# Kernel tuning notes

Hardware: AMD Instinct MI355X
Metric: run time of the kernel (lower is better)

Reference implementation:

```python
import jax, jax.numpy as jnp
import numpy as np

B, S, D, H, M = 4, 2048, 1024, 16, 128
DH = D // H
SCALE = jnp.float32(np.sqrt(D / H))


def setup_inputs() -> dict:
    key = jax.random.key(0)
    ks = jax.random.split(key, 4)
    x = jax.random.normal(ks[0], (B, S, D), dtype=jnp.float32)
    mask = jnp.zeros((B, 1, 1, S), dtype=bool)
    W_in = jax.random.normal(ks[1], (3 * D, D), dtype=jnp.float32) * 0.02
    b_in = jnp.zeros((3 * D,), dtype=jnp.float32)
    pos_emb = jax.random.normal(ks[2], (2 * M + 1, DH), dtype=jnp.float32)
    W_out = jax.random.normal(ks[3], (D, D), dtype=jnp.float32) * 0.02
    b_out = jnp.zeros((D,), dtype=jnp.float32)
    return {"x": x, "mask": mask, "W_in": W_in, "b_in": b_in,
            "pos_emb": pos_emb, "W_out": W_out, "b_out": b_out}


def _arrange_pos(pos_emb, seq_len, max_len):
    k = jnp.arange(seq_len)
    q = jnp.arange(seq_len)
    idx = jnp.clip(k[None, :] - q[:, None], -max_len, max_len) + max_len  # [S,S]
    return pos_emb[idx]  # [S,S,DH]


def reference(x, mask, W_in, b_in, pos_emb, W_out, b_out):
    b, s, d = x.shape
    qkv = x @ W_in.T + b_in                      # [B,S,3D]
    qkv = qkv.reshape(b, s, H, 3 * DH).transpose(0, 2, 1, 3)  # [B,H,S,3DH]
    Q, K, V = jnp.split(qkv, 3, axis=3)          # each [B,H,S,DH]
    logits = jnp.einsum('bhqd,bhkd->bhqk', Q, K)
    rel = _arrange_pos(pos_emb, s, M)            # [S,S,DH] (q,k,dh)
    pos_logits = jnp.einsum('bhqd,qkd->bhqk', Q, rel)
    logits = (logits + pos_logits) / SCALE
    logits = jnp.where(mask, -jnp.inf, logits)
    attn = jax.nn.softmax(logits, axis=3)
    combined = jnp.einsum('bhqk,bhkd->bhqd', attn, V)
    out = combined.transpose(0, 2, 1, 3).reshape(b, s, d)  # concat heads
    return out @ W_out.T + b_out
```

## Files before the change

### kernel.cpp

```cpp
#include <hip/hip_runtime.h>
#include <hip/hip_bf16.h>
#include <math.h>

#define SS 2048
#define HH 16
#define NPOS 257
#define C_SCALE 0.18033688f
#define DTHR 8.0f

typedef short  s16x8 __attribute__((ext_vector_type(8)));
typedef float  f32x4 __attribute__((ext_vector_type(4)));
typedef unsigned u32x4 __attribute__((ext_vector_type(4)));

__device__ __forceinline__ unsigned short f2bf(float f) {
    unsigned u = __builtin_bit_cast(unsigned, f);
    u += 0x7fff + ((u >> 16) & 1);
    return (unsigned short)(u >> 16);
}
__device__ __forceinline__ float bf2f(unsigned short b) {
    return __builtin_bit_cast(float, (unsigned)b << 16);
}
__device__ __forceinline__ s16x8 pack8(float4 a, float4 b) {
    s16x8 v;
    v[0]=(short)f2bf(a.x); v[1]=(short)f2bf(a.y); v[2]=(short)f2bf(a.z); v[3]=(short)f2bf(a.w);
    v[4]=(short)f2bf(b.x); v[5]=(short)f2bf(b.y); v[6]=(short)f2bf(b.z); v[7]=(short)f2bf(b.w);
    return v;
}
__device__ __forceinline__ unsigned cvtpk(float lo, float hi) {
    unsigned r;
    asm("v_cvt_pk_bf16_f32 %0, %1, %2" : "=v"(r) : "v"(lo), "v"(hi));
    return r;
}
__device__ __forceinline__ float exp2_fast(float x) {
    float r;
    asm("v_exp_f32 %0, %1" : "=v"(r) : "v"(x));
    return r;
}
__device__ __forceinline__ f32x4 mfma16(s16x8 a, s16x8 b, f32x4 c) {
    return __builtin_amdgcn_mfma_f32_16x16x32_bf16(a, b, c, 0, 0, 0);
}
__device__ __forceinline__ void gload_lds16(const void* gsrc, void* ldst) {
    __builtin_amdgcn_global_load_lds(
        (const __attribute__((address_space(1))) unsigned int*)gsrc,
        (__attribute__((address_space(3))) unsigned int*)ldst,
        16, 0, 0);
}
__device__ __forceinline__ int colp(int k) {
    return ((k >> 5) << 6) | (((k >> 2) & 3) << 4) | (((k >> 4) & 1) << 3) | ((k & 3) << 1);
}

__global__ __launch_bounds__(256)
void cvt_bf16(const float* __restrict__ in, unsigned short* __restrict__ out, int n8)
{
    for (int i = blockIdx.x * blockDim.x + threadIdx.x; i < n8; i += gridDim.x * blockDim.x) {
        const float4* p = (const float4*)(in + (size_t)i * 8);
        *(s16x8*)(out + (size_t)i * 8) = pack8(p[0], p[1]);
    }
}

__global__ __launch_bounds__(256)
void gemm_bf16_nt(const unsigned short* __restrict__ A,
                  const unsigned short* __restrict__ Bm,
                  const float* __restrict__ bias, void* __restrict__ Cout,
                  int Ndim, int Kdim, int out_bf16)
{
    __shared__ short As[128 * 32];
    __shared__ short Bs[128 * 32];
    const int tid  = threadIdx.x;
    const int lane = tid & 63;
    const int wv   = tid >> 6;
    const int g    = lane >> 4;
    const int ln   = lane & 15;
    const int wm   = wv >> 1, wn = wv & 1;
    const int tm   = blockIdx.y << 7, tn = blockIdx.x << 7;
    const int srow  = lane >> 2;
    const int sslot = lane & 3;

    f32x4 acc[4][4];
#pragma unroll
    for (int mi = 0; mi < 4; ++mi)
#pragma unroll
        for (int ni = 0; ni < 4; ++ni) acc[mi][ni] = f32x4{0.f, 0.f, 0.f, 0.f};

    const unsigned short* Ab = A  + (size_t)(tm + wv*32 + srow) * Kdim + sslot*8;
    const unsigned short* Bb = Bm + (size_t)(tn + wv*32 + srow) * Kdim + sslot*8;
    const size_t rstep16 = (size_t)16 * Kdim;
    char* lA = (char*)As + (wv*32) * 64;
    char* lB = (char*)Bs + (wv*32) * 64;

    for (int k0 = 0; k0 < Kdim; k0 += 32) {
        __syncthreads();
        gload_lds16(Ab + k0,           lA);
        gload_lds16(Ab + k0 + rstep16, lA + 1024);
        gload_lds16(Bb + k0,           lB);
        gload_lds16(Bb + k0 + rstep16, lB + 1024);
        __syncthreads();

        s16x8 af[4], bf_[4];
#pragma unroll
        for (int mi = 0; mi < 4; ++mi)
            af[mi] = *(const s16x8*)((char*)As + (wm*64 + mi*16 + ln)*64 + g*16);
#pragma unroll
        for (int ni = 0; ni < 4; ++ni)
            bf_[ni] = *(const s16x8*)((char*)Bs + (wn*64 + ni*16 + ln)*64 + g*16);
#pragma unroll
        for (int mi = 0; mi < 4; ++mi)
#pragma unroll
            for (int ni = 0; ni < 4; ++ni)
                acc[mi][ni] = mfma16(af[mi], bf_[ni], acc[mi][ni]);
    }

#pragma unroll
    for (int ni = 0; ni < 4; ++ni) {
        const int col = tn + wn*64 + ni*16 + ln;
        const float bcol = bias[col];
#pragma unroll
        for (int mi = 0; mi < 4; ++mi) {
#pragma unroll
            for (int j = 0; j < 4; ++j) {
                const int row = tm + wm*64 + mi*16 + 4*g + j;
                const float v = acc[mi][ni][j] + bcol;
                if (out_bf16) ((unsigned short*)Cout)[(size_t)row * Ndim + col] = f2bf(v);
                else          ((float*)Cout)[(size_t)row * Ndim + col] = v;
            }
        }
    }
}

#define FAR_LDS  32768
#define NEAR_LDS (32768 + 64*260*2)

#define QKT_STEP(kbp)                                                         \
    f32x4 sA[4], sB[4];                                                       \
    _Pragma("unroll")                                                         \
    for (int t = 0; t < 4; ++t) { sA[t] = f32x4{0,0,0,0}; sB[t] = f32x4{0,0,0,0}; } \
    __builtin_amdgcn_s_setprio(1);                                            \
    _Pragma("unroll")                                                         \
    for (int kc = 0; kc < 2; ++kc) {                                          \
        s16x8 kf[4];                                                          \
        _Pragma("unroll")                                                     \
        for (int t = 0; t < 4; ++t)                                           \
            kf[t] = *(const s16x8*)((kbp) + (t*16 + ln)*128 + ((kc*64 + g*16) ^ swz)); \
        _Pragma("unroll")                                                     \
        for (int t = 0; t < 4; ++t) {                                         \
            sA[t] = mfma16(kf[t], qfA[kc], sA[t]);                            \
            sB[t] = mfma16(kf[t], qfB[kc], sB[t]);                            \
        }                                                                     \
    }                                                                         \
    __builtin_amdgcn_s_setprio(0);

#define SOFTMAX_AV(vbp)                                                       \
    {                                                                         \
        float mxA = sA[0][0], mxB = sB[0][0];                                 \
        _Pragma("unroll")                                                     \
        for (int t = 0; t < 4; ++t)                                           \
            _Pragma("unroll")                                                 \
            for (int j = 0; j < 4; ++j) {                                     \
                mxA = fmaxf(mxA, sA[t][j]); mxB = fmaxf(mxB, sB[t][j]);       \
            }                                                                 \
        if (__any(fmaxf(mxA - mA, mxB - mB) > DTHR)) {                        \
            float mrA = mxA, mrB = mxB;                                       \
            mrA = fmaxf(mrA, __shfl_xor(mrA, 16, 64));                        \
            mrA = fmaxf(mrA, __shfl_xor(mrA, 32, 64));                        \
            mrB = fmaxf(mrB, __shfl_xor(mrB, 16, 64));                        \
            mrB = fmaxf(mrB, __shfl_xor(mrB, 32, 64));                        \
            const float nmA = fmaxf(mA, mrA), nmB = fmaxf(mB, mrB);           \
            const float cA = exp2_fast(mA - nmA), cB = exp2_fast(mB - nmB);   \
            mA = nmA; mB = nmB;                                               \
            _Pragma("unroll")                                                 \
            for (int j = 0; j < 4; ++j) {                                     \
                const int src = (lane & 48) + 4*g + j;                        \
                const float aj = __shfl(cA, src, 64), bj = __shfl(cB, src, 64); \
                _Pragma("unroll")                                             \
                for (int dt = 0; dt < 4; ++dt) { oA[dt][j] *= aj; oB[dt][j] *= bj; } \
                lA[j] *= aj; lB[j] *= bj;                                     \
            }                                                                 \
        }                                                                     \
        u32x4 paA[2], paB[2];                                                 \
        _Pragma("unroll")                                                     \
        for (int t = 0; t < 4; ++t) {                                         \
            const float a0 = exp2_fast(sA[t][0] - mA), a1 = exp2_fast(sA[t][1] - mA); \
            const float a2 = exp2_fast(sA[t][2] - mA), a3 = exp2_fast(sA[t][3] - mA); \
            const float b0 = exp2_fast(sB[t][0] - mB), b1 = exp2_fast(sB[t][1] - mB); \
            const float b2 = exp2_fast(sB[t][2] - mB), b3 = exp2_fast(sB[t][3] - mB); \
            paA[t>>1][2*(t&1)]   = cvtpk(a0, a1);                             \
            paA[t>>1][2*(t&1)+1] = cvtpk(a2, a3);                             \
            paB[t>>1][2*(t&1)]   = cvtpk(b0, b1);                             \
            paB[t>>1][2*(t&1)+1] = cvtpk(b2, b3);                             \
        }                                                                     \
        __builtin_amdgcn_s_setprio(1);                                        \
        _Pragma("unroll")                                                     \
        for (int kc = 0; kc < 2; ++kc) {                                      \
            const s16x8 pA_ = __builtin_bit_cast(s16x8, paA[kc]);             \
            const s16x8 pB_ = __builtin_bit_cast(s16x8, paB[kc]);             \
            _Pragma("unroll")                                                 \
            for (int dt = 0; dt < 4; ++dt) {                                  \
                const s16x8 bv = *(const s16x8*)((vbp) + (dt*16 + ln)*128 + ((kc*64 + g*16) ^ swz)); \
                oA[dt] = mfma16(pA_, bv, oA[dt]);                             \
                oB[dt] = mfma16(pB_, bv, oB[dt]);                             \
            }                                                                 \
            lA = mfma16(pA_, ONES, lA);                                       \
            lB = mfma16(pB_, ONES, lB);                                       \
        }                                                                     \
        __builtin_amdgcn_s_setprio(0);                                        \
    }

#define WRITE_V_PAIR(vb_, vlo, vhi, dbase)                                    \
    _Pragma("unroll")                                                         \
    for (int c_ = 0; c_ < 8; ++c_) {                                          \
        const int d_ = (dbase) + c_;                                          \
        const unsigned pv_ = (unsigned)(unsigned short)(vlo)[c_] |            \
                             ((unsigned)(unsigned short)(vhi)[c_] << 16);     \
        *(unsigned*)((vb_) + d_*128 + (vcp ^ ((d_&7)<<4))) = pv_;             \
    }

__global__ __launch_bounds__(256, 3)
void attn_far(const unsigned short* __restrict__ qkv,
              const float* __restrict__ pos_emb,
              float* __restrict__ o_state,
              float* __restrict__ m_state,
              float* __restrict__ l_state)
{
    extern __shared__ char smem[];
    char* ksb = smem;
    char* vtb = smem + 16384;

    const int tid = threadIdx.x, lane = tid & 63, wv = tid >> 6;
    const int g = lane >> 4, ln = lane & 15;
    const int fid = ((blockIdx.x & 7) << 7) | (blockIdx.x >> 3);
    const int q0 = (fid & 15) << 7, h = (fid >> 4) & 15, b = fid >> 8;
    const size_t base = ((size_t)b * SS) * 3072 + (size_t)h * 192;
    const int q0w = q0 + wv*32;
    const int swz = (ln & 7) << 4;

    s16x8 qfA[2], qfB[2];
    {
        const unsigned short* qp = qkv + base + (size_t)(q0w + ln) * 3072;
        qfA[0] = *(const s16x8*)(qp + g*8);
        qfA[1] = *(const s16x8*)(qp + 32 + g*8);
        qp += (size_t)16 * 3072;
        qfB[0] = *(const s16x8*)(qp + g*8);
        qfB[1] = *(const s16x8*)(qp + 32 + g*8);
    }

    const int kdof = 8*((lane & 7) ^ (lane >> 3));
    const unsigned short* kgp0 = qkv + base + 64 + (size_t)(16*wv + (lane>>3)) * 3072 + kdof;
    const unsigned short* kgp1 = kgp0 + (size_t)8*3072;
    char* kld = ksb + wv*2048;
    const int vs  = tid & 31;
    const int vdc = (tid >> 5) << 3;
    const int vcp = colp(2*vs);
    const unsigned short* vg0 = qkv + base + 128 + (size_t)(2*vs) * 3072 + vdc;
    const unsigned short* vg1 = vg0 + 3072;
    s16x8 vK0, vK1;

#define F_ISSUE_K(kt, buf) do {                                               \
        gload_lds16(kgp0 + (size_t)(kt)*(64*3072), kld + (buf)*8192);         \
        gload_lds16(kgp1 + (size_t)(kt)*(64*3072), kld + (buf)*8192 + 1024); } while (0)
#define F_ISSUE_V(kt) do {                                                    \
        vK0 = *(const s16x8*)(vg0 + (size_t)(kt)*(64*3072));                  \
        vK1 = *(const s16x8*)(vg1 + (size_t)(kt)*(64*3072)); } while (0)

    const int ktA = max(0, (q0 - 128) >> 6);
    const int ktB = min(32, (q0 + 256) >> 6);
    const int gap = ktB - ktA, nfar = 32 - gap;

    {
        const int kt0 = (0 < ktA) ? 0 : gap;
        F_ISSUE_K(kt0, 0);
        F_ISSUE_V(kt0);
    }

    float bloA, bhiA, bloB, bhiB;
    {
        const int bsrc = (ln >> 2) << 4;
#pragma unroll
        for (int pass = 0; pass < 2; ++pass) {
            const int c  = pass*256 + ln;
            const int cc = c > 256 ? 256 : c;
            const float* pp = pos_emb + (size_t)cc * 64 + 8*g;
            s16x8 b0 = pack8(((const float4*)pp)[0], ((const float4*)(pp+4))[0]);
            s16x8 b1 = pack8(((const float4*)(pp+32))[0], ((const float4*)(pp+36))[0]);
            f32x4 dA = {0,0,0,0}, dB = {0,0,0,0};
            dA = mfma16(qfA[0], b0, dA); dA = mfma16(qfA[1], b1, dA);
            dB = mfma16(qfB[0], b0, dB); dB = mfma16(qfB[1], b1, dB);
            const int s3 = ln & 3;
            float vA_ = __shfl(dA[0]*C_SCALE, bsrc, 64);
            float vA1 = __shfl(dA[1]*C_SCALE, bsrc, 64);
            float vA2 = __shfl(dA[2]*C_SCALE, bsrc, 64);
            float vA3 = __shfl(dA[3]*C_SCALE, bsrc, 64);
            float rA = s3 == 0 ? vA_ : s3 == 1 ? vA1 : s3 == 2 ? vA2 : vA3;
            float vB_ = __shfl(dB[0]*C_SCALE, bsrc, 64);
            float vB1 = __shfl(dB[1]*C_SCALE, bsrc, 64);
            float vB2 = __shfl(dB[2]*C_SCALE, bsrc, 64);
            float vB3 = __shfl(dB[3]*C_SCALE, bsrc, 64);
            float rB = s3 == 0 ? vB_ : s3 == 1 ? vB1 : s3 == 2 ? vB2 : vB3;
            if (pass == 0) { bloA = rA; bloB = rB; } else { bhiA = rA; bhiB = rB; }
        }
    }

    WRITE_V_PAIR(vtb, vK0, vK1, vdc)
    __syncthreads();

    f32x4 oA[4], oB[4], lA = {0,0,0,0}, lB = {0,0,0,0};
#pragma unroll
    for (int dt = 0; dt < 4; ++dt) { oA[dt] = f32x4{0,0,0,0}; oB[dt] = f32x4{0,0,0,0}; }
    float mA = -INFINITY, mB = -INFINITY;
    s16x8 ONES;
#pragma unroll
    for (int i = 0; i < 8; ++i) ONES[i] = (short)0x3F80;

    for (int v = 0; v < nfar; ++v) {
        const int kt = (v < ktA) ? v : v + gap;
        const char* kbp = ksb + (v & 1)*8192;
        const char* vbp = vtb + (v & 1)*8192;
        if (v + 1 < nfar) {
            const int ktn = (v + 1 < ktA) ? v + 1 : v + 1 + gap;
            F_ISSUE_K(ktn, (v + 1) & 1);
            F_ISSUE_V(ktn);
        }

        QKT_STEP(kbp)

        const float bcA = (kt < ktA) ? bloA : bhiA;
        const float bcB = (kt < ktA) ? bloB : bhiB;
#pragma unroll
        for (int t = 0; t < 4; ++t)
#pragma unroll
            for (int j = 0; j < 4; ++j) {
                sA[t][j] = sA[t][j]*C_SCALE + bcA;
                sB[t][j] = sB[t][j]*C_SCALE + bcB;
            }

        SOFTMAX_AV(vbp)

        if (v + 1 < nfar) WRITE_V_PAIR(vtb + ((v+1)&1)*8192, vK0, vK1, vdc)
        __syncthreads();
    }

    const size_t rbase = (((size_t)(b*HH + h)) << 11) + q0w;
    if (lane < 16)      m_state[rbase + ln] = mA;
    else if (lane < 32) m_state[rbase + 16 + ln] = mB;
    if (ln == 0) {
#pragma unroll
        for (int j = 0; j < 4; ++j) l_state[rbase + 4*g + j] = lA[j];
    } else if (ln == 1) {
#pragma unroll
        for (int j = 0; j < 4; ++j) l_state[rbase + 16 + 4*g + j] = lB[j];
    }
#pragma unroll
    for (int dt = 0; dt < 4; ++dt)
#pragma unroll
        for (int j = 0; j < 4; ++j) {
            o_state[(rbase + 4*g + j)*64 + dt*16 + ln]      = oA[dt][j];
            o_state[(rbase + 16 + 4*g + j)*64 + dt*16 + ln] = oB[dt][j];
        }
}

__global__ __launch_bounds__(128)
void attn_near(const unsigned short* __restrict__ qkv,
               const float* __restrict__ pos_emb,
               const float* __restrict__ o_state,
               const float* __restrict__ m_state,
               const float* __restrict__ l_state,
               unsigned short* __restrict__ comb)
{
    extern __shared__ char smem[];
    char* ksb = smem;
    char* vtb = smem + 16384;
    unsigned short* tab = (unsigned short*)(smem + 32768);

    const int tid = threadIdx.x, lane = tid & 63, wv = tid >> 6;
    const int g = lane >> 4, ln = lane & 15;
    const int fid = ((blockIdx.x & 7) << 8) | (blockIdx.x >> 3);
    const int q0 = (fid & 31) << 6, h = (fid >> 5) & 15, b = fid >> 9;
    const size_t base = ((size_t)b * SS) * 3072 + (size_t)h * 192;
    const int q0w = q0 + wv*32;
    const int swz = (ln & 7) << 4;

    s16x8 qfA[2], qfB[2];
    {
        const unsigned short* qp = qkv + base + (size_t)(q0w + ln) * 3072;
        qfA[0] = *(const s16x8*)(qp + g*8);
        qfA[1] = *(const s16x8*)(qp + 32 + g*8);
        qp += (size_t)16 * 3072;
        qfB[0] = *(const s16x8*)(qp + g*8);
        qfB[1] = *(const s16x8*)(qp + 32 + g*8);
    }

    const int kdof = 8*((lane & 7) ^ (lane >> 3));
    const unsigned short* kgpN = qkv + base + 64 + (size_t)(32*wv + (lane>>3)) * 3072 + kdof;
    char* kldN = ksb + wv*4096;
    const int vs  = tid & 31;
    const int vdc = (tid >> 5) << 3;
    const int vcp = colp(2*vs);
    const unsigned short* vg0 = qkv + base + 128 + (size_t)(2*vs) * 3072 + vdc;
    const unsigned short* vg1 = vg0 + 3072;
    s16x8 vA0, vA1, vB0, vB1;

#define N_ISSUE_K(kt, buf) do {                                               \
        _Pragma("unroll")                                                     \
        for (int gs = 0; gs < 4; ++gs)                                        \
            gload_lds16(kgpN + (size_t)(kt)*(64*3072) + (size_t)gs*(8*3072),  \
                        kldN + (buf)*8192 + gs*1024); } while (0)
#define N_ISSUE_V(kt) do {                                                    \
        vA0 = *(const s16x8*)(vg0 + (size_t)(kt)*(64*3072));                  \
        vA1 = *(const s16x8*)(vg1 + (size_t)(kt)*(64*3072));                  \
        vB0 = *(const s16x8*)(vg0 + (size_t)(kt)*(64*3072) + 32);             \
        vB1 = *(const s16x8*)(vg1 + (size_t)(kt)*(64*3072) + 32); } while (0)
#define N_WRITE_V(buf) do {                                                   \
        char* vb_ = vtb + (buf)*8192;                                         \
        WRITE_V_PAIR(vb_, vA0, vA1, vdc)                                      \
        WRITE_V_PAIR(vb_, vB0, vB1, vdc + 32)                                 \
    } while (0)

    const int q0p = q0 & ~127;
    const int ktA = max(0, (q0p - 128) >> 6);
    const int ktB = min(32, (q0p + 256) >> 6);
    const int ntile = ktB - ktA;

    N_ISSUE_K(ktA, 0);
    N_ISSUE_V(ktA);

    for (int ct = 0; ct < 17; ++ct) {
        const int c  = ct*16 + ln;
        const int cc = c > 256 ? 256 : c;
        const float* pp = pos_emb + (size_t)cc * 64 + 8*g;
        s16x8 b0 = pack8(((const float4*)pp)[0], ((const float4*)(pp+4))[0]);
        s16x8 b1 = pack8(((const float4*)(pp+32))[0], ((const float4*)(pp+36))[0]);
        f32x4 dA = {0,0,0,0}, dB = {0,0,0,0};
        dA = mfma16(qfA[0], b0, dA); dA = mfma16(qfA[1], b1, dA);
        dB = mfma16(qfB[0], b0, dB); dB = mfma16(qfB[1], b1, dB);
        if (c < NPOS) {
#pragma unroll
            for (int j = 0; j < 4; ++j) {
                tab[(32*wv + 4*g + j)*260 + c]      = f2bf(dA[j] * C_SCALE);
                tab[(32*wv + 16 + 4*g + j)*260 + c] = f2bf(dB[j] * C_SCALE);
            }
        }
    }

    N_WRITE_V(0);
    __syncthreads();

    const size_t rbase = (((size_t)(b*HH + h)) << 11) + q0w;
    float mA = m_state[rbase + ln];
    float mB = m_state[rbase + 16 + ln];
    f32x4 lA, lB;
#pragma unroll
    for (int j = 0; j < 4; ++j) {
        lA[j] = l_state[rbase + 4*g + j];
        lB[j] = l_state[rbase + 16 + 4*g + j];
    }
    f32x4 oA[4], oB[4];
#pragma unroll
    for (int dt = 0; dt < 4; ++dt)
#pragma unroll
        for (int j = 0; j < 4; ++j) {
            oA[dt][j] = o_state[(rbase + 4*g + j)*64 + dt*16 + ln];
            oB[dt][j] = o_state[(rbase + 16 + 4*g + j)*64 + dt*16 + ln];
        }

    const int rowA = (32*wv + ln)*260, rowB = rowA + 16*260;
    const int coffA = 4*g - 32*wv - ln + 128 - q0;
    const int coffB = coffA - 16;
    s16x8 ONES;
#pragma unroll
    for (int i = 0; i < 8; ++i) ONES[i] = (short)0x3F80;

    for (int v = 0; v < ntile; ++v) {
        const int kt = ktA + v;
        const char* kbp = ksb + (v & 1)*8192;
        const char* vbp = vtb + (v & 1)*8192;
        if (v + 1 < ntile) { N_ISSUE_K(kt + 1, (v + 1) & 1); N_ISSUE_V(kt + 1); }

        QKT_STEP(kbp)

        const int kb0 = kt << 6;
#pragma unroll
        for (int t = 0; t < 4; ++t)
#pragma unroll
            for (int j = 0; j < 4; ++j) {
                int cA = kb0 + 16*t + j + coffA;
                cA = cA < 0 ? 0 : (cA > 256 ? 256 : cA);
                int cB = kb0 + 16*t + j + coffB;
                cB = cB < 0 ? 0 : (cB > 256 ? 256 : cB);
                sA[t][j] = sA[t][j]*C_SCALE + bf2f(tab[rowA + cA]);
                sB[t][j] = sB[t][j]*C_SCALE + bf2f(tab[rowB + cB]);
            }

        SOFTMAX_AV(vbp)

        if (v + 1 < ntile) N_WRITE_V((v + 1) & 1);
        __syncthreads();
    }

    f32x4 ivA, ivB;
#pragma unroll
    for (int j = 0; j < 4; ++j) { ivA[j] = 1.0f / lA[j]; ivB[j] = 1.0f / lB[j]; }
#pragma unroll
    for (int dt = 0; dt < 4; ++dt)
#pragma unroll
        for (int j = 0; j < 4; ++j) {
            comb[((size_t)b*SS + q0w + 4*g + j)*1024 + h*64 + dt*16 + ln] =
                f2bf(oA[dt][j] * ivA[j]);
            comb[((size_t)b*SS + q0w + 16 + 4*g + j)*1024 + h*64 + dt*16 + ln] =
                f2bf(oB[dt][j] * ivB[j]);
        }
}

extern "C" void kernel_launch(void* const* d_in, const int* in_sizes, int n_in,
                              void* d_out, int out_size, void* d_ws, size_t ws_size,
                              hipStream_t stream)
{
    const float* x     = (const float*)d_in[0];
    const float* W_in  = (const float*)d_in[2];
    const float* b_in  = (const float*)d_in[3];
    const float* pos   = (const float*)d_in[4];
    const float* W_out = (const float*)d_in[5];
    const float* b_out = (const float*)d_in[6];
    float* out = (float*)d_out;

    char* ws = (char*)d_ws;
    unsigned short* qkv_bf  = (unsigned short*)(ws);
    unsigned short* comb_bf = (unsigned short*)(ws +  50331648);
    unsigned short* x_bf    = (unsigned short*)(ws +  67108864);
    unsigned short* wi_bf   = (unsigned short*)(ws +  83886080);
    unsigned short* wo_bf   = (unsigned short*)(ws +  90177536);
    float*          o_state = (float*)        (ws +  92274688);
    float*          m_state = (float*)        (ws + 125829120);
    float*          l_state = (float*)        (ws + 126353408);

    cvt_bf16<<<2048, 256, 0, stream>>>(x,     x_bf,  8192*1024/8);
    cvt_bf16<<<1024, 256, 0, stream>>>(W_in,  wi_bf, 3072*1024/8);
    cvt_bf16<<<512,  256, 0, stream>>>(W_out, wo_bf, 1024*1024/8);

    gemm_bf16_nt<<<dim3(24, 64), 256, 0, stream>>>(x_bf, wi_bf, b_in, qkv_bf, 3072, 1024, 1);

    (void)hipFuncSetAttribute((const void*)attn_far,
                              hipFuncAttributeMaxDynamicSharedMemorySize, FAR_LDS);
    attn_far<<<dim3(1024), 256, FAR_LDS, stream>>>(qkv_bf, pos, o_state, m_state, l_state);

    (void)hipFuncSetAttribute((const void*)attn_near,
                              hipFuncAttributeMaxDynamicSharedMemorySize, NEAR_LDS);
    attn_near<<<dim3(2048), 128, NEAR_LDS, stream>>>(qkv_bf, pos, o_state, m_state, l_state, comb_bf);

    gemm_bf16_nt<<<dim3(8, 64), 256, 0, stream>>>(comb_bf, wo_bf, b_out, (void*)out, 1024, 1024, 0);
}
```

Measured before the change: 300.0 us.

## Rebalance attention warps: far kernel 64 rows/warp, near kernel 16 rows/warp

The far-attention kernel now runs 2 waves per block, each owning 64 query rows (four 16-row groups). Each K/V fragment loaded from LDS is therefore reused across four MFMA groups, and each wave issues four K loads and four V loads. The near kernel goes the other way: 4 waves per block with 16 rows each, which lowers register pressure and the per-wave work inside the band. The trade-off is higher register use and lower occupancy in the far kernel (launch bounds 128,2) in exchange for better LDS reuse, plus more waves per block and more synchronization in the near kernel.

```diff
diff --git a/kernel.cpp b/kernel.cpp
--- a/kernel.cpp
+++ b/kernel.cpp
@@ -130,81 +130,6 @@
 #define FAR_LDS  32768
 #define NEAR_LDS (32768 + 64*260*2)
 
-#define QKT_STEP(kbp)                                                         \
-    f32x4 sA[4], sB[4];                                                       \
-    _Pragma("unroll")                                                         \
-    for (int t = 0; t < 4; ++t) { sA[t] = f32x4{0,0,0,0}; sB[t] = f32x4{0,0,0,0}; } \
-    __builtin_amdgcn_s_setprio(1);                                            \
-    _Pragma("unroll")                                                         \
-    for (int kc = 0; kc < 2; ++kc) {                                          \
-        s16x8 kf[4];                                                          \
-        _Pragma("unroll")                                                     \
-        for (int t = 0; t < 4; ++t)                                           \
-            kf[t] = *(const s16x8*)((kbp) + (t*16 + ln)*128 + ((kc*64 + g*16) ^ swz)); \
-        _Pragma("unroll")                                                     \
-        for (int t = 0; t < 4; ++t) {                                         \
-            sA[t] = mfma16(kf[t], qfA[kc], sA[t]);                            \
-            sB[t] = mfma16(kf[t], qfB[kc], sB[t]);                            \
-        }                                                                     \
-    }                                                                         \
-    __builtin_amdgcn_s_setprio(0);
-
-#define SOFTMAX_AV(vbp)                                                       \
-    {                                                                         \
-        float mxA = sA[0][0], mxB = sB[0][0];                                 \
-        _Pragma("unroll")                                                     \
-        for (int t = 0; t < 4; ++t)                                           \
-            _Pragma("unroll")                                                 \
-            for (int j = 0; j < 4; ++j) {                                     \
-                mxA = fmaxf(mxA, sA[t][j]); mxB = fmaxf(mxB, sB[t][j]);       \
-            }                                                                 \
-        if (__any(fmaxf(mxA - mA, mxB - mB) > DTHR)) {                        \
-            float mrA = mxA, mrB = mxB;                                       \
-            mrA = fmaxf(mrA, __shfl_xor(mrA, 16, 64));                        \
-            mrA = fmaxf(mrA, __shfl_xor(mrA, 32, 64));                        \
-            mrB = fmaxf(mrB, __shfl_xor(mrB, 16, 64));                        \
-            mrB = fmaxf(mrB, __shfl_xor(mrB, 32, 64));                        \
-            const float nmA = fmaxf(mA, mrA), nmB = fmaxf(mB, mrB);           \
-            const float cA = exp2_fast(mA - nmA), cB = exp2_fast(mB - nmB);   \
-            mA = nmA; mB = nmB;                                               \
-            _Pragma("unroll")                                                 \
-            for (int j = 0; j < 4; ++j) {                                     \
-                const int src = (lane & 48) + 4*g + j;                        \
-                const float aj = __shfl(cA, src, 64), bj = __shfl(cB, src, 64); \
-                _Pragma("unroll")                                             \
-                for (int dt = 0; dt < 4; ++dt) { oA[dt][j] *= aj; oB[dt][j] *= bj; } \
-                lA[j] *= aj; lB[j] *= bj;                                     \
-            }                                                                 \
-        }                                                                     \
-        u32x4 paA[2], paB[2];                                                 \
-        _Pragma("unroll")                                                     \
-        for (int t = 0; t < 4; ++t) {                                         \
-            const float a0 = exp2_fast(sA[t][0] - mA), a1 = exp2_fast(sA[t][1] - mA); \
-            const float a2 = exp2_fast(sA[t][2] - mA), a3 = exp2_fast(sA[t][3] - mA); \
-            const float b0 = exp2_fast(sB[t][0] - mB), b1 = exp2_fast(sB[t][1] - mB); \
-            const float b2 = exp2_fast(sB[t][2] - mB), b3 = exp2_fast(sB[t][3] - mB); \
-            paA[t>>1][2*(t&1)]   = cvtpk(a0, a1);                             \
-            paA[t>>1][2*(t&1)+1] = cvtpk(a2, a3);                             \
-            paB[t>>1][2*(t&1)]   = cvtpk(b0, b1);                             \
-            paB[t>>1][2*(t&1)+1] = cvtpk(b2, b3);                             \
-        }                                                                     \
-        __builtin_amdgcn_s_setprio(1);                                        \
-        _Pragma("unroll")                                                     \
-        for (int kc = 0; kc < 2; ++kc) {                                      \
-            const s16x8 pA_ = __builtin_bit_cast(s16x8, paA[kc]);             \
-            const s16x8 pB_ = __builtin_bit_cast(s16x8, paB[kc]);             \
-            _Pragma("unroll")                                                 \
-            for (int dt = 0; dt < 4; ++dt) {                                  \
-                const s16x8 bv = *(const s16x8*)((vbp) + (dt*16 + ln)*128 + ((kc*64 + g*16) ^ swz)); \
-                oA[dt] = mfma16(pA_, bv, oA[dt]);                             \
-                oB[dt] = mfma16(pB_, bv, oB[dt]);                             \
-            }                                                                 \
-            lA = mfma16(pA_, ONES, lA);                                       \
-            lB = mfma16(pB_, ONES, lB);                                       \
-        }                                                                     \
-        __builtin_amdgcn_s_setprio(0);                                        \
-    }
-
 #define WRITE_V_PAIR(vb_, vlo, vhi, dbase)                                    \
     _Pragma("unroll")                                                         \
     for (int c_ = 0; c_ < 8; ++c_) {                                          \
@@ -214,7 +139,7 @@
         *(unsigned*)((vb_) + d_*128 + (vcp ^ ((d_&7)<<4))) = pv_;             \
     }
 
-__global__ __launch_bounds__(256, 3)
+__global__ __launch_bounds__(128, 2)
 void attn_far(const unsigned short* __restrict__ qkv,
               const float* __restrict__ pos_emb,
               float* __restrict__ o_state,
@@ -230,36 +155,42 @@
     const int fid = ((blockIdx.x & 7) << 7) | (blockIdx.x >> 3);
     const int q0 = (fid & 15) << 7, h = (fid >> 4) & 15, b = fid >> 8;
     const size_t base = ((size_t)b * SS) * 3072 + (size_t)h * 192;
-    const int q0w = q0 + wv*32;
+    const int q0w = q0 + wv*64;
     const int swz = (ln & 7) << 4;
 
-    s16x8 qfA[2], qfB[2];
-    {
-        const unsigned short* qp = qkv + base + (size_t)(q0w + ln) * 3072;
-        qfA[0] = *(const s16x8*)(qp + g*8);
-        qfA[1] = *(const s16x8*)(qp + 32 + g*8);
-        qp += (size_t)16 * 3072;
-        qfB[0] = *(const s16x8*)(qp + g*8);
-        qfB[1] = *(const s16x8*)(qp + 32 + g*8);
+    s16x8 qf[4][2];
+#pragma unroll
+    for (int gg = 0; gg < 4; ++gg) {
+        const unsigned short* qp = qkv + base + (size_t)(q0w + 16*gg + ln) * 3072;
+        qf[gg][0] = *(const s16x8*)(qp + g*8);
+        qf[gg][1] = *(const s16x8*)(qp + 32 + g*8);
     }
 
     const int kdof = 8*((lane & 7) ^ (lane >> 3));
-    const unsigned short* kgp0 = qkv + base + 64 + (size_t)(16*wv + (lane>>3)) * 3072 + kdof;
-    const unsigned short* kgp1 = kgp0 + (size_t)8*3072;
-    char* kld = ksb + wv*2048;
+    const unsigned short* kgp0 = qkv + base + 64 + (size_t)(32*wv + (lane>>3)) * 3072 + kdof;
+    char* kld = ksb + wv*4096;
     const int vs  = tid & 31;
     const int vdc = (tid >> 5) << 3;
     const int vcp = colp(2*vs);
     const unsigned short* vg0 = qkv + base + 128 + (size_t)(2*vs) * 3072 + vdc;
     const unsigned short* vg1 = vg0 + 3072;
-    s16x8 vK0, vK1;
+    s16x8 vK0, vK1, vK2, vK3;
 
 #define F_ISSUE_K(kt, buf) do {                                               \
-        gload_lds16(kgp0 + (size_t)(kt)*(64*3072), kld + (buf)*8192);         \
-        gload_lds16(kgp1 + (size_t)(kt)*(64*3072), kld + (buf)*8192 + 1024); } while (0)
+        _Pragma("unroll")                                                     \
+        for (int gs = 0; gs < 4; ++gs)                                        \
+            gload_lds16(kgp0 + (size_t)(kt)*(64*3072) + (size_t)gs*(8*3072),  \
+                        kld + (buf)*8192 + gs*1024); } while (0)
 #define F_ISSUE_V(kt) do {                                                    \
-        vK0 = *(const s16x8*)(vg0 + (size_t)(kt)*(64*3072));                  \
-        vK1 = *(const s16x8*)(vg1 + (size_t)(kt)*(64*3072)); } while (0)
+        const unsigned short* v0_ = vg0 + (size_t)(kt)*(64*3072);             \
+        const unsigned short* v1_ = vg1 + (size_t)(kt)*(64*3072);             \
+        vK0 = *(const s16x8*)(v0_);      vK1 = *(const s16x8*)(v1_);          \
+        vK2 = *(const s16x8*)(v0_ + 32); vK3 = *(const s16x8*)(v1_ + 32); } while (0)
+#define F_WRITE_V(buf) do {                                                   \
+        char* vb_ = vtb + (buf)*8192;                                         \
+        WRITE_V_PAIR(vb_, vK0, vK1, vdc)                                      \
+        WRITE_V_PAIR(vb_, vK2, vK3, vdc + 32)                                 \
+    } while (0)
 
     const int ktA = max(0, (q0 - 128) >> 6);
     const int ktB = min(32, (q0 + 256) >> 6);
@@ -271,9 +202,10 @@
         F_ISSUE_V(kt0);
     }
 
-    float bloA, bhiA, bloB, bhiB;
+    float blo[4], bhi[4];
     {
         const int bsrc = (ln >> 2) << 4;
+        const int s3 = ln & 3;
 #pragma unroll
         for (int pass = 0; pass < 2; ++pass) {
             const int c  = pass*256 + ln;
@@ -281,31 +213,32 @@
             const float* pp = pos_emb + (size_t)cc * 64 + 8*g;
             s16x8 b0 = pack8(((const float4*)pp)[0], ((const float4*)(pp+4))[0]);
             s16x8 b1 = pack8(((const float4*)(pp+32))[0], ((const float4*)(pp+36))[0]);
-            f32x4 dA = {0,0,0,0}, dB = {0,0,0,0};
-            dA = mfma16(qfA[0], b0, dA); dA = mfma16(qfA[1], b1, dA);
-            dB = mfma16(qfB[0], b0, dB); dB = mfma16(qfB[1], b1, dB);
-            const int s3 = ln & 3;
-            float vA_ = __shfl(dA[0]*C_SCALE, bsrc, 64);
-            float vA1 = __shfl(dA[1]*C_SCALE, bsrc, 64);
-            float vA2 = __shfl(dA[2]*C_SCALE, bsrc, 64);
-            float vA3 = __shfl(dA[3]*C_SCALE, bsrc, 64);
-            float rA = s3 == 0 ? vA_ : s3 == 1 ? vA1 : s3 == 2 ? vA2 : vA3;
-            float vB_ = __shfl(dB[0]*C_SCALE, bsrc, 64);
-            float vB1 = __shfl(dB[1]*C_SCALE, bsrc, 64);
-            float vB2 = __shfl(dB[2]*C_SCALE, bsrc, 64);
-            float vB3 = __shfl(dB[3]*C_SCALE, bsrc, 64);
-            float rB = s3 == 0 ? vB_ : s3 == 1 ? vB1 : s3 == 2 ? vB2 : vB3;
-            if (pass == 0) { bloA = rA; bloB = rB; } else { bhiA = rA; bhiB = rB; }
-        }
-    }
-
-    WRITE_V_PAIR(vtb, vK0, vK1, vdc)
+#pragma unroll
+            for (int gg = 0; gg < 4; ++gg) {
+                f32x4 d = {0,0,0,0};
+                d = mfma16(qf[gg][0], b0, d);
+                d = mfma16(qf[gg][1], b1, d);
+                const float r0 = __shfl(d[0]*C_SCALE, bsrc, 64);
+                const float r1 = __shfl(d[1]*C_SCALE, bsrc, 64);
+                const float r2 = __shfl(d[2]*C_SCALE, bsrc, 64);
+                const float r3 = __shfl(d[3]*C_SCALE, bsrc, 64);
+                const float r = s3 == 0 ? r0 : s3 == 1 ? r1 : s3 == 2 ? r2 : r3;
+                if (pass == 0) blo[gg] = r; else bhi[gg] = r;
+            }
+        }
+    }
+
+    F_WRITE_V(0);
     __syncthreads();
 
-    f32x4 oA[4], oB[4], lA = {0,0,0,0}, lB = {0,0,0,0};
-#pragma unroll
-    for (int dt = 0; dt < 4; ++dt) { oA[dt] = f32x4{0,0,0,0}; oB[dt] = f32x4{0,0,0,0}; }
-    float mA = -INFINITY, mB = -INFINITY;
+    f32x4 o[4][4], l[4];
+    float m[4];
+#pragma unroll
+    for (int gg = 0; gg < 4; ++gg) {
+        m[gg] = -INFINITY; l[gg] = f32x4{0,0,0,0};
+#pragma unroll
+        for (int dt = 0; dt < 4; ++dt) o[gg][dt] = f32x4{0,0,0,0};
+    }
     s16x8 ONES;
 #pragma unroll
     for (int i = 0; i < 8; ++i) ONES[i] = (short)0x3F80;
@@ -320,44 +253,115 @@
             F_ISSUE_V(ktn);
         }
 
-        QKT_STEP(kbp)
-
-        const float bcA = (kt < ktA) ? bloA : bhiA;
-        const float bcB = (kt < ktA) ? bloB : bhiB;
-#pragma unroll
-        for (int t = 0; t < 4; ++t)
-#pragma unroll
-            for (int j = 0; j < 4; ++j) {
-                sA[t][j] = sA[t][j]*C_SCALE + bcA;
-                sB[t][j] = sB[t][j]*C_SCALE + bcB;
-            }
-
-        SOFTMAX_AV(vbp)
-
-        if (v + 1 < nfar) WRITE_V_PAIR(vtb + ((v+1)&1)*8192, vK0, vK1, vdc)
+        u32x4 pa[4][2];
+#pragma unroll
+        for (int hf = 0; hf < 2; ++hf) {
+            f32x4 s[2][4];
+#pragma unroll
+            for (int gi = 0; gi < 2; ++gi)
+#pragma unroll
+                for (int t = 0; t < 4; ++t) s[gi][t] = f32x4{0,0,0,0};
+            __builtin_amdgcn_s_setprio(1);
+#pragma unroll
+            for (int kc = 0; kc < 2; ++kc) {
+                s16x8 kf[4];
+#pragma unroll
+                for (int t = 0; t < 4; ++t)
+                    kf[t] = *(const s16x8*)(kbp + (t*16 + ln)*128 + ((kc*64 + g*16) ^ swz));
+#pragma unroll
+                for (int t = 0; t < 4; ++t)
+#pragma unroll
+                    for (int gi = 0; gi < 2; ++gi)
+                        s[gi][t] = mfma16(kf[t], qf[2*hf + gi][kc], s[gi][t]);
+            }
+            __builtin_amdgcn_s_setprio(0);
+
+            float mx[2];
+#pragma unroll
+            for (int gi = 0; gi < 2; ++gi) {
+                const int gg = 2*hf + gi;
+                const float bc = (kt < ktA) ? blo[gg] : bhi[gg];
+                float m0 = -INFINITY;
+#pragma unroll
+                for (int t = 0; t < 4; ++t)
+#pragma unroll
+                    for (int j = 0; j < 4; ++j) {
+                        s[gi][t][j] = s[gi][t][j]*C_SCALE + bc;
+                        m0 = fmaxf(m0, s[gi][t][j]);
+                    }
+                mx[gi] = m0;
+            }
+            if (__any(fmaxf(mx[0] - m[2*hf], mx[1] - m[2*hf+1]) > DTHR)) {
+#pragma unroll
+                for (int gi = 0; gi < 2; ++gi) {
+                    const int gg = 2*hf + gi;
+                    float mr = mx[gi];
+                    mr = fmaxf(mr, __shfl_xor(mr, 16, 64));
+                    mr = fmaxf(mr, __shfl_xor(mr, 32, 64));
+                    const float nm = fmaxf(m[gg], mr);
+                    const float corr = exp2_fast(m[gg] - nm);
+                    m[gg] = nm;
+#pragma unroll
+                    for (int j = 0; j < 4; ++j) {
+                        const float cj = __shfl(corr, (lane & 48) + 4*g + j, 64);
+#pragma unroll
+                        for (int dt = 0; dt < 4; ++dt) o[gg][dt][j] *= cj;
+                        l[gg][j] *= cj;
+                    }
+                }
+            }
+#pragma unroll
+            for (int gi = 0; gi < 2; ++gi) {
+                const int gg = 2*hf + gi;
+#pragma unroll
+                for (int t = 0; t < 4; ++t) {
+                    const float p0 = exp2_fast(s[gi][t][0] - m[gg]);
+                    const float p1 = exp2_fast(s[gi][t][1] - m[gg]);
+                    const float p2 = exp2_fast(s[gi][t][2] - m[gg]);
+                    const float p3 = exp2_fast(s[gi][t][3] - m[gg]);
+                    pa[gg][t>>1][2*(t&1)]   = cvtpk(p0, p1);
+                    pa[gg][t>>1][2*(t&1)+1] = cvtpk(p2, p3);
+                }
+            }
+        }
+
+        __builtin_amdgcn_s_setprio(1);
+#pragma unroll
+        for (int kc = 0; kc < 2; ++kc) {
+#pragma unroll
+            for (int dt = 0; dt < 4; ++dt) {
+                const s16x8 bv = *(const s16x8*)(vbp + (dt*16 + ln)*128 + ((kc*64 + g*16) ^ swz));
+#pragma unroll
+                for (int gg = 0; gg < 4; ++gg)
+                    o[gg][dt] = mfma16(__builtin_bit_cast(s16x8, pa[gg][kc]), bv, o[gg][dt]);
+            }
+#pragma unroll
+            for (int gg = 0; gg < 4; ++gg)
+                l[gg] = mfma16(__builtin_bit_cast(s16x8, pa[gg][kc]), ONES, l[gg]);
+        }
+        __builtin_amdgcn_s_setprio(0);
+
+        if (v + 1 < nfar) F_WRITE_V((v + 1) & 1);
         __syncthreads();
     }
 
     const size_t rbase = (((size_t)(b*HH + h)) << 11) + q0w;
-    if (lane < 16)      m_state[rbase + ln] = mA;
-    else if (lane < 32) m_state[rbase + 16 + ln] = mB;
-    if (ln == 0) {
-#pragma unroll
-        for (int j = 0; j < 4; ++j) l_state[rbase + 4*g + j] = lA[j];
-    } else if (ln == 1) {
-#pragma unroll
-        for (int j = 0; j < 4; ++j) l_state[rbase + 16 + 4*g + j] = lB[j];
-    }
-#pragma unroll
-    for (int dt = 0; dt < 4; ++dt)
-#pragma unroll
-        for (int j = 0; j < 4; ++j) {
-            o_state[(rbase + 4*g + j)*64 + dt*16 + ln]      = oA[dt][j];
-            o_state[(rbase + 16 + 4*g + j)*64 + dt*16 + ln] = oB[dt][j];
-        }
-}
-
-__global__ __launch_bounds__(128)
+#pragma unroll
+    for (int gg = 0; gg < 4; ++gg) {
+        if (lane < 16) m_state[rbase + 16*gg + ln] = m[gg];
+        if (ln == 0) {
+#pragma unroll
+            for (int j = 0; j < 4; ++j) l_state[rbase + 16*gg + 4*g + j] = l[gg][j];
+        }
+#pragma unroll
+        for (int dt = 0; dt < 4; ++dt)
+#pragma unroll
+            for (int j = 0; j < 4; ++j)
+                o_state[(rbase + 16*gg + 4*g + j)*64 + dt*16 + ln] = o[gg][dt][j];
+    }
+}
+
+__global__ __launch_bounds__(256, 2)
 void attn_near(const unsigned short* __restrict__ qkv,
                const float* __restrict__ pos_emb,
                const float* __restrict__ o_state,
@@ -375,43 +379,36 @@
     const int fid = ((blockIdx.x & 7) << 8) | (blockIdx.x >> 3);
     const int q0 = (fid & 31) << 6, h = (fid >> 5) & 15, b = fid >> 9;
     const size_t base = ((size_t)b * SS) * 3072 + (size_t)h * 192;
-    const int q0w = q0 + wv*32;
+    const int q0w = q0 + wv*16;
     const int swz = (ln & 7) << 4;
 
-    s16x8 qfA[2], qfB[2];
+    s16x8 qf[2];
     {
         const unsigned short* qp = qkv + base + (size_t)(q0w + ln) * 3072;
-        qfA[0] = *(const s16x8*)(qp + g*8);
-        qfA[1] = *(const s16x8*)(qp + 32 + g*8);
-        qp += (size_t)16 * 3072;
-        qfB[0] = *(const s16x8*)(qp + g*8);
-        qfB[1] = *(const s16x8*)(qp + 32 + g*8);
+        qf[0] = *(const s16x8*)(qp + g*8);
+        qf[1] = *(const s16x8*)(qp + 32 + g*8);
     }
 
     const int kdof = 8*((lane & 7) ^ (lane >> 3));
-    const unsigned short* kgpN = qkv + base + 64 + (size_t)(32*wv + (lane>>3)) * 3072 + kdof;
-    char* kldN = ksb + wv*4096;
+    const unsigned short* kgp0 = qkv + base + 64 + (size_t)(16*wv + (lane>>3)) * 3072 + kdof;
+    char* kld = ksb + wv*2048;
     const int vs  = tid & 31;
     const int vdc = (tid >> 5) << 3;
     const int vcp = colp(2*vs);
     const unsigned short* vg0 = qkv + base + 128 + (size_t)(2*vs) * 3072 + vdc;
     const unsigned short* vg1 = vg0 + 3072;
-    s16x8 vA0, vA1, vB0, vB1;
+    s16x8 vK0, vK1;
 
 #define N_ISSUE_K(kt, buf) do {                                               \
-        _Pragma("unroll")                                                     \
-        for (int gs = 0; gs < 4; ++gs)                                        \
-            gload_lds16(kgpN + (size_t)(kt)*(64*3072) + (size_t)gs*(8*3072),  \
-                        kldN + (buf)*8192 + gs*1024); } while (0)
+        gload_lds16(kgp0 + (size_t)(kt)*(64*3072), kld + (buf)*8192);         \
+        gload_lds16(kgp0 + (size_t)(kt)*(64*3072) + (size_t)(8*3072),         \
+                    kld + (buf)*8192 + 1024); } while (0)
 #define N_ISSUE_V(kt) do {                                                    \
-        vA0 = *(const s16x8*)(vg0 + (size_t)(kt)*(64*3072));                  \
-        vA1 = *(const s16x8*)(vg1 + (size_t)(kt)*(64*3072));                  \
-        vB0 = *(const s16x8*)(vg0 + (size_t)(kt)*(64*3072) + 32);             \
-        vB1 = *(const s16x8*)(vg1 + (size_t)(kt)*(64*3072) + 32); } while (0)
+        vK0 = *(const s16x8*)(vg0 + (size_t)(kt)*(64*3072));                  \
+        vK1 = *(const s16x8*)(vg1 + (size_t)(kt)*(64*3072)); } while (0)
 #define N_WRITE_V(buf) do {                                                   \
         char* vb_ = vtb + (buf)*8192;                                         \
-        WRITE_V_PAIR(vb_, vA0, vA1, vdc)                                      \
-        WRITE_V_PAIR(vb_, vB0, vB1, vdc + 32)                                 \
+        WRITE_V_PAIR(vb_, vK0, vK1, vdc)                                      \
     } while (0)
 
     const int q0p = q0 & ~127;
@@ -428,15 +425,13 @@
         const float* pp = pos_emb + (size_t)cc * 64 + 8*g;
         s16x8 b0 = pack8(((const float4*)pp)[0], ((const float4*)(pp+4))[0]);
         s16x8 b1 = pack8(((const float4*)(pp+32))[0], ((const float4*)(pp+36))[0]);
-        f32x4 dA = {0,0,0,0}, dB = {0,0,0,0};
-        dA = mfma16(qfA[0], b0, dA); dA = mfma16(qfA[1], b1, dA);
-        dB = mfma16(qfB[0], b0, dB); dB = mfma16(qfB[1], b1, dB);
+        f32x4 d = {0,0,0,0};
+        d = mfma16(qf[0], b0, d);
+        d = mfma16(qf[1], b1, d);
         if (c < NPOS) {
 #pragma unroll
-            for (int j = 0; j < 4; ++j) {
-                tab[(32*wv + 4*g + j)*260 + c]      = f2bf(dA[j] * C_SCALE);
-                tab[(32*wv + 16 + 4*g + j)*260 + c] = f2bf(dB[j] * C_SCALE);
-            }
+            for (int j = 0; j < 4; ++j)
+                tab[(16*wv + 4*g + j)*260 + c] = f2bf(d[j] * C_SCALE);
         }
     }
 
@@ -444,26 +439,19 @@
     __syncthreads();
 
     const size_t rbase = (((size_t)(b*HH + h)) << 11) + q0w;
-    float mA = m_state[rbase + ln];
-    float mB = m_state[rbase + 16 + ln];
-    f32x4 lA, lB;
-#pragma unroll
-    for (int j = 0; j < 4; ++j) {
-        lA[j] = l_state[rbase + 4*g + j];
-        lB[j] = l_state[rbase + 16 + 4*g + j];
-    }
-    f32x4 oA[4], oB[4];
+    float m_run = m_state[rbase + ln];
+    f32x4 l_acc;
+#pragma unroll
+    for (int j = 0; j < 4; ++j) l_acc[j] = l_state[rbase + 4*g + j];
+    f32x4 o_acc[4];
 #pragma unroll
     for (int dt = 0; dt < 4; ++dt)
 #pragma unroll
-        for (int j = 0; j < 4; ++j) {
-            oA[dt][j] = o_state[(rbase + 4*g + j)*64 + dt*16 + ln];
-            oB[dt][j] = o_state[(rbase + 16 + 4*g + j)*64 + dt*16 + ln];
-        }
-
-    const int rowA = (32*wv + ln)*260, rowB = rowA + 16*260;
-    const int coffA = 4*g - 32*wv - ln + 128 - q0;
-    const int coffB = coffA - 16;
+        for (int j = 0; j < 4; ++j)
+            o_acc[dt][j] = o_state[(rbase + 4*g + j)*64 + dt*16 + ln];
+
+    const int rowb = (16*wv + ln) * 260;
+    const int coff = 4*g - 16*wv - ln + 128 - q0;
     s16x8 ONES;
 #pragma unroll
     for (int i = 0; i < 8; ++i) ONES[i] = (short)0x3F80;
@@ -474,39 +462,87 @@
         const char* vbp = vtb + (v & 1)*8192;
         if (v + 1 < ntile) { N_ISSUE_K(kt + 1, (v + 1) & 1); N_ISSUE_V(kt + 1); }
 
-        QKT_STEP(kbp)
-
-        const int kb0 = kt << 6;
+        f32x4 s[4];
+#pragma unroll
+        for (int t = 0; t < 4; ++t) s[t] = f32x4{0,0,0,0};
+        __builtin_amdgcn_s_setprio(1);
+#pragma unroll
+        for (int kc = 0; kc < 2; ++kc) {
+            s16x8 kf[4];
+#pragma unroll
+            for (int t = 0; t < 4; ++t)
+                kf[t] = *(const s16x8*)(kbp + (t*16 + ln)*128 + ((kc*64 + g*16) ^ swz));
+#pragma unroll
+            for (int t = 0; t < 4; ++t)
+                s[t] = mfma16(kf[t], qf[kc], s[t]);
+        }
+        __builtin_amdgcn_s_setprio(0);
+
+        const int colb = (kt << 6) + coff;
+        float mx = -INFINITY;
 #pragma unroll
         for (int t = 0; t < 4; ++t)
 #pragma unroll
             for (int j = 0; j < 4; ++j) {
-                int cA = kb0 + 16*t + j + coffA;
-                cA = cA < 0 ? 0 : (cA > 256 ? 256 : cA);
-                int cB = kb0 + 16*t + j + coffB;
-                cB = cB < 0 ? 0 : (cB > 256 ? 256 : cB);
-                sA[t][j] = sA[t][j]*C_SCALE + bf2f(tab[rowA + cA]);
-                sB[t][j] = sB[t][j]*C_SCALE + bf2f(tab[rowB + cB]);
-            }
-
-        SOFTMAX_AV(vbp)
+                int c = colb + 16*t + j;
+                c = c < 0 ? 0 : (c > 256 ? 256 : c);
+                s[t][j] = s[t][j]*C_SCALE + bf2f(tab[rowb + c]);
+                mx = fmaxf(mx, s[t][j]);
+            }
+
+        if (__any(mx > m_run + DTHR)) {
+            float mr = mx;
+            mr = fmaxf(mr, __shfl_xor(mr, 16, 64));
+            mr = fmaxf(mr, __shfl_xor(mr, 32, 64));
+            const float nm = fmaxf(m_run, mr);
+            const float corr = exp2_fast(m_run - nm);
+            m_run = nm;
+#pragma unroll
+            for (int j = 0; j < 4; ++j) {
+                const float cj = __shfl(corr, (lane & 48) + 4*g + j, 64);
+#pragma unroll
+                for (int dt = 0; dt < 4; ++dt) o_acc[dt][j] *= cj;
+                l_acc[j] *= cj;
+            }
+        }
+
+        u32x4 pa[2];
+#pragma unroll
+        for (int t = 0; t < 4; ++t) {
+            const float p0 = exp2_fast(s[t][0] - m_run);
+            const float p1 = exp2_fast(s[t][1] - m_run);
+            const float p2 = exp2_fast(s[t][2] - m_run);
+            const float p3 = exp2_fast(s[t][3] - m_run);
+            pa[t>>1][2*(t&1)]   = cvtpk(p0, p1);
+            pa[t>>1][2*(t&1)+1] = cvtpk(p2, p3);
+        }
+
+        __builtin_amdgcn_s_setprio(1);
+#pragma unroll
+        for (int kc = 0; kc < 2; ++kc) {
+            const s16x8 pA_ = __builtin_bit_cast(s16x8, pa[kc]);
+#pragma unroll
+            for (int dt = 0; dt < 4; ++dt) {
+                const s16x8 bv = *(const s16x8*)(vbp + (dt*16 + ln)*128 + ((kc*64 + g*16) ^ swz));
+                o_acc[dt] = mfma16(pA_, bv, o_acc[dt]);
+            }
+            l_acc = mfma16(pA_, ONES, l_acc);
+        }
+        __builtin_amdgcn_s_setprio(0);
 
         if (v + 1 < ntile) N_WRITE_V((v + 1) & 1);
         __syncthreads();
     }
 
-    f32x4 ivA, ivB;
-#pragma unroll
-    for (int j = 0; j < 4; ++j) { ivA[j] = 1.0f / lA[j]; ivB[j] = 1.0f / lB[j]; }
+    f32x4 inv;
+#pragma unroll
+    for (int j = 0; j < 4; ++j) inv[j] = 1.0f / l_acc[j];
 #pragma unroll
     for (int dt = 0; dt < 4; ++dt)
 #pragma unroll
-        for (int j = 0; j < 4; ++j) {
+        for (int j = 0; j < 4; ++j)
             comb[((size_t)b*SS + q0w + 4*g + j)*1024 + h*64 + dt*16 + ln] =
-                f2bf(oA[dt][j] * ivA[j]);
-            comb[((size_t)b*SS + q0w + 16 + 4*g + j)*1024 + h*64 + dt*16 + ln] =
-                f2bf(oB[dt][j] * ivB[j]);
-        }
+                f2bf(o_acc[dt][j] * inv[j]);
 }
 
 extern "C" void kernel_launch(void* const* d_in, const int* in_sizes, int n_in,
@@ -539,11 +575,11 @@
 
     (void)hipFuncSetAttribute((const void*)attn_far,
                               hipFuncAttributeMaxDynamicSharedMemorySize, FAR_LDS);
-    attn_far<<<dim3(1024), 256, FAR_LDS, stream>>>(qkv_bf, pos, o_state, m_state, l_state);
+    attn_far<<<dim3(1024), 128, FAR_LDS, stream>>>(qkv_bf, pos, o_state, m_state, l_state);
 
     (void)hipFuncSetAttribute((const void*)attn_near,
                               hipFuncAttributeMaxDynamicSharedMemorySize, NEAR_LDS);
-    attn_near<<<dim3(2048), 128, NEAR_LDS, stream>>>(qkv_bf, pos, o_state, m_state, l_state, comb_bf);
+    attn_near<<<dim3(2048), 256, NEAR_LDS, stream>>>(qkv_bf, pos, o_state, m_state, l_state, comb_bf);
 
     gemm_bf16_nt<<<dim3(8, 64), 256, 0, stream>>>(comb_bf, wo_bf, b_out, (void*)out, 1024, 1024, 0);
 }
```

Result: no change. 303.8 us (+1.3%).
